# Kernel optimization log

Hardware: AMD Instinct MI355X
Metric: run time of the kernel (lower is better)

The kernel has to match this reference:

```python
import jax, jax.numpy as jnp
import numpy as np

# ---- constants matching init_kwargs ----
NUM_CLASSES = 20
NUM_GRID = 7
NUM_BBOX = 2
IN_SIZE = 448          # image_shapes = (448, 448)
IOU_THRESHOLD = 0.7    # self.num_threshold passed to batched_nms
SCORE_THRESHOLD = 0.1  # boxes[:, -1] > 0.1 reserve mask
M = NUM_GRID * NUM_GRID  # 49 boxes per image
BATCH = 16384


def setup_inputs() -> dict:
    key = jax.random.key(0)
    out_features = M * (NUM_CLASSES + 5 * NUM_BBOX)  # 1470
    x = jax.random.uniform(key, (BATCH, out_features), dtype=jnp.float32)
    return {"x": x}


def _iou_matrix(boxes):
    # boxes: [M, 4] in (x0, y0, x1, y1). Returns [M, M] pairwise IoU.
    area = jnp.clip(boxes[:, 2] - boxes[:, 0], 0) * jnp.clip(boxes[:, 3] - boxes[:, 1], 0)
    lt = jnp.maximum(boxes[:, None, :2], boxes[None, :, :2])   # [M, M, 2]
    rb = jnp.minimum(boxes[:, None, 2:], boxes[None, :, 2:])   # [M, M, 2]
    wh = jnp.clip(rb - lt, 0)
    inter = wh[..., 0] * wh[..., 1]
    union = area[:, None] + area[None, :] - inter
    return inter / jnp.maximum(union, 1e-9)


def _nms_keep(boxes, scores, labels, valid):
    # Per-image class-aware NMS (torchvision batched_nms semantics via coordinate offsets).
    # boxes [M,4], scores [M], labels [M] int, valid [M] bool -> keep mask [M] bool.
    max_coord = jnp.max(boxes)
    offs = labels.astype(boxes.dtype) * (max_coord + 1.0)
    b = boxes + offs[:, None]
    s = jnp.where(valid, scores, -jnp.inf)
    order = jnp.argsort(-s)                 # descending by score, invalid last
    bs = b[order]
    vs = valid[order]
    iou = _iou_matrix(bs)                   # [M, M]
    idx = jnp.arange(M)

    def step(suppressed, i):
        keep_i = vs[i] & ~suppressed[i]
        suppressed = suppressed | (keep_i & (iou[i] > IOU_THRESHOLD) & (idx > i))
        return suppressed, keep_i

    _, keep_sorted = jax.lax.scan(step, jnp.zeros((M,), bool), idx)
    return jnp.zeros((M,), bool).at[order].set(keep_sorted)


def reference(x):
    N = x.shape[0]
    x = x.reshape(N, M, NUM_CLASSES + 5 * NUM_BBOX)
    class_logits = x[..., :NUM_CLASSES]                       # [N, M, C]
    bb = x[..., NUM_CLASSES:].reshape(N, M, NUM_BBOX, 5)      # [N, M, B, 5]
    # pick the bbox with max confidence per cell
    best = jnp.argmax(bb[..., 4], axis=-1)                    # [N, M]
    yolo_bboxes = jnp.take_along_axis(bb, best[..., None, None], axis=2)[:, :, 0, :]  # [N, M, 5]

    probs = jax.nn.softmax(class_logits, axis=-1)
    labels = jnp.argmax(probs, axis=-1)                       # [N, M]

    # boxes_decode: grid offsets (x tiles, y repeats) then cx/cy/w/h -> corners
    g = jnp.arange(NUM_GRID, dtype=x.dtype)
    x_grid = jnp.tile(g, NUM_GRID)                            # [M]
    y_grid = jnp.repeat(g, NUM_GRID)                          # [M]
    cx = (yolo_bboxes[..., 0] + x_grid) / NUM_GRID
    cy = (yolo_bboxes[..., 1] + y_grid) / NUM_GRID
    hw = yolo_bboxes[..., 2] / 2
    hh = yolo_bboxes[..., 3] / 2
    W = jnp.asarray(IN_SIZE, x.dtype)
    H = jnp.asarray(IN_SIZE, x.dtype)
    x0 = (cx - hw) * W
    y0 = (cy - hh) * H
    x1 = (cx + hw) * W
    y1 = (cy + hh) * H
    scores = yolo_bboxes[..., 4]
    reserve_mask = scores > SCORE_THRESHOLD                   # [N, M]

    # clip_boxes_to_image
    x0 = jnp.clip(x0, 0, IN_SIZE); x1 = jnp.clip(x1, 0, IN_SIZE)
    y0 = jnp.clip(y0, 0, IN_SIZE); y1 = jnp.clip(y1, 0, IN_SIZE)
    boxes = jnp.stack([x0, y0, x1, y1], axis=-1)              # [N, M, 4]

    keep_mask = jax.vmap(_nms_keep)(boxes, scores, labels, reserve_mask)  # [N, M]
    return class_logits, yolo_bboxes, boxes, scores, labels, keep_mask, reserve_mask
```

## Files before the change

### kernel.cpp

```cpp
#include <hip/hip_runtime.h>
#include <math.h>

#define NCLS   20
#define MCELLS 49
#define FEAT   30
#define ITEMF  1470

typedef unsigned long long u64;
typedef unsigned int u32;
typedef float f32x4 __attribute__((ext_vector_type(4)));

__device__ __forceinline__ int bcasti(int v, int l) {
  return __builtin_amdgcn_readlane(v, l);
}
__device__ __forceinline__ void nts(float* p, float v) { __builtin_nontemporal_store(v, p); }

__global__ __launch_bounds__(256) void yolo_post(const float* __restrict__ x,
                                                 float* __restrict__ out,
                                                 int N) {
  const int wave = threadIdx.x >> 6;
  const int lane = threadIdx.x & 63;
  const int n = blockIdx.x * 4 + wave;
  if (n >= N) return;

  const float* item = x + (size_t)n * ITEMF;

  const size_t NM = (size_t)N * MCELLS;
  float* out0 = out;
  float* out1 = out0 + NM * 20;
  float* out2 = out1 + NM * 5;
  float* out3 = out2 + NM * 4;
  float* out4 = out3 + NM;
  float* out5 = out4 + NM;
  float* out6 = out5 + NM;

  const int m = lane;
  const bool cellv = (m < MCELLS);

  float2 v[15];
  if (cellv) {
    const float2* Lp = (const float2*)(item + m * FEAT);
#pragma unroll
    for (int j = 0; j < 15; ++j) v[j] = Lp[j];
  } else {
#pragma unroll
    for (int j = 0; j < 15; ++j) v[j] = make_float2(0.f, 0.f);
  }

  {
    float* dst = out0 + (size_t)n * (MCELLS * NCLS);
#pragma unroll
    for (int i = 0; i < 16; ++i) {
      int idx = lane + i * 64;
      if (idx < MCELLS * NCLS) {
        int c = idx / NCLS;
        int k = idx - c * NCLS;
        nts(dst + idx, item[c * FEAT + k]);
      }
    }
  }

  int   labi = 0;
  float conf = 0.f;
  float x0 = 0.f, y0 = 0.f, x1 = 0.f, y1 = 0.f;
  bool  reserve = false;

  if (cellv) {
    float bestv = v[0].x;
    if (v[0].y > bestv) { bestv = v[0].y; labi = 1; }
#pragma unroll
    for (int j = 1; j < 10; ++j) {
      if (v[j].x > bestv) { bestv = v[j].x; labi = 2 * j; }
      if (v[j].y > bestv) { bestv = v[j].y; labi = 2 * j + 1; }
    }

    float c0 = v[12].x, c1 = v[14].y;
    bool sel1 = (c1 > c0);
    float bx = sel1 ? v[12].y : v[10].x;
    float by = sel1 ? v[13].x : v[10].y;
    float bw = sel1 ? v[13].y : v[11].x;
    float bh = sel1 ? v[14].x : v[11].y;
    conf = sel1 ? c1 : c0;

    float xg = (float)(m % 7), yg = (float)(m / 7);
    float cx = (bx + xg) / 7.0f, cy = (by + yg) / 7.0f;
    float hw = bw * 0.5f, hh = bh * 0.5f;
    x0 = fminf(fmaxf((cx - hw) * 448.0f, 0.f), 448.f);
    y0 = fminf(fmaxf((cy - hh) * 448.0f, 0.f), 448.f);
    x1 = fminf(fmaxf((cx + hw) * 448.0f, 0.f), 448.f);
    y1 = fminf(fmaxf((cy + hh) * 448.0f, 0.f), 448.f);
    reserve = (conf > 0.1f);

    size_t ci = (size_t)n * MCELLS + m;
    float* yb = out1 + ci * 5;
    nts(yb + 0, bx); nts(yb + 1, by); nts(yb + 2, bw); nts(yb + 3, bh); nts(yb + 4, conf);
    f32x4 bx4 = { x0, y0, x1, y1 };
    __builtin_nontemporal_store(bx4, (f32x4*)(out2 + ci * 4));
    nts(out3 + ci, conf);
    nts(out4 + ci, (float)labi);
    nts(out6 + ci, reserve ? 1.0f : 0.0f);
  }

  u64 key;
  if (cellv && reserve) {
    u32 sb = __float_as_uint(conf);
    u32 inv = 0x7FFFFFFFu - sb;
    key = ((u64)labi << 37) | ((u64)inv << 6) | (u64)lane;
  } else {
    key = ~0ull;
  }

#pragma unroll
  for (int k = 2; k <= 64; k <<= 1) {
#pragma unroll
    for (int j = k >> 1; j >= 1; j >>= 1) {
      u64 ok = __shfl(key, lane ^ j);
      bool lower = (lane & j) == 0;
      bool asc = (lane & k) == 0;
      if ((key > ok) == (lower == asc)) key = ok;
    }
  }

  const int sid  = (int)(key & 63);
  const int slab = (int)((key >> 37) & 31);

  float gx0 = __shfl(x0, sid), gy0 = __shfl(y0, sid);
  float gx1 = __shfl(x1, sid), gy1 = __shfl(y1, sid);
  float garea = fmaxf(gx1 - gx0, 0.f) * fmaxf(gy1 - gy0, 0.f);

  {
  }
  int prevlab = __shfl(slab, (lane + 63) & 63);
  bool rstart = (lane == 0) || (prevlab != slab);
  u64 S = __ballot(rstart);
  u64 le_mask = (lane == 63) ? ~0ull : ((2ull << lane) - 1ull);
  int st = 63 - __builtin_clzll(S & le_mask);
  u64 gt = (lane == 63) ? 0ull : (S >> (lane + 1));
  int nxt = gt ? (lane + 1 + (int)__builtin_ctzll(gt)) : 64;
  int rl = (slab != 31) ? (nxt - st) : 1;
#pragma unroll
  for (int d2 = 1; d2 < 64; d2 <<= 1) {
    int o = __shfl_xor(rl, d2);
    rl = rl > o ? rl : o;
  }
  const int Dmax = __builtin_amdgcn_readfirstlane(rl);

  u64 rowm = 0;
  for (int d = 1; d < Dmax; ++d) {
    int srcl = (lane + d) & 63;
    int plab = __shfl(slab, srcl);
    float px0 = __shfl(gx0, srcl), py0 = __shfl(gy0, srcl);
    float px1 = __shfl(gx1, srcl), py1 = __shfl(gy1, srcl);
    float pa  = __shfl(garea, srcl);
    bool match = (plab == slab) && (slab != 31) && (lane + d < 64);
    float iw = fmaxf(fminf(px1, gx1) - fmaxf(px0, gx0), 0.f);
    float ih = fmaxf(fminf(py1, gy1) - fmaxf(py0, gy0), 0.f);
    float inter = iw * ih;
    float uni = pa + garea - inter;
    bool ok = match && (inter > 0.7f * fmaxf(uni, 1e-9f));
    rowm |= ok ? (1ull << srcl) : 0ull;
  }

  int V = __popcll(__ballot(key != ~0ull));
  int rlo = (int)(rowm & 0xFFFFFFFFull), rhi = (int)(rowm >> 32);
  u64 remaining = (V >= 64) ? ~0ull : ((1ull << V) - 1ull);
  u64 keep = 0;
  while (remaining) {
    int i = (int)__builtin_ctzll(remaining);
    keep |= 1ull << i;
    u64 rm = ((u64)(u32)bcasti(rhi, i) << 32) | (u32)bcasti(rlo, i);
    remaining &= ~(rm | (1ull << i));
  }

  int kb = (int)((keep >> lane) & 1ull);
  int kf = __builtin_amdgcn_ds_permute(sid << 2, __float_as_int((float)kb));
  if (cellv) nts(out5 + (size_t)n * MCELLS + m, __int_as_float(kf));
}

extern "C" void kernel_launch(void* const* d_in, const int* in_sizes, int n_in,
                              void* d_out, int out_size, void* d_ws, size_t ws_size,
                              hipStream_t stream) {
  const float* x = (const float*)d_in[0];
  float* out = (float*)d_out;
  int N = in_sizes[0] / ITEMF;
  int grid = (N + 3) / 4;
  yolo_post<<<grid, 256, 0, stream>>>(x, out, N);
}
```

Measured before the change: 43.09 us.

## Replace bitonic sort NMS with LDS-based all-pairs suppression and ballot resolution

Drops the 64-lane bitonic sort and sorted-order serial NMS loop. Instead, each lane writes its box and metadata to LDS, tests all 49 boxes for same-class higher-score overlap to build a candidate suppressor mask, and resolves keep decisions with a wave-wide iterative ballot that stops once no undecided boxes remain. This removes the shuffle-heavy sort and the per-kept readlane chain, at the cost of 49 LDS reads per lane and a loop whose iteration count depends on the length of the suppression dependency chain.

Result: slower. 54.72 us (+27.0%).

```diff
diff --git a/kernel.cpp b/kernel.cpp
--- a/kernel.cpp
+++ b/kernel.cpp
@@ -10,9 +10,6 @@
 typedef unsigned int u32;
 typedef float f32x4 __attribute__((ext_vector_type(4)));
 
-__device__ __forceinline__ int bcasti(int v, int l) {
-  return __builtin_amdgcn_readlane(v, l);
-}
 __device__ __forceinline__ void nts(float* p, float v) { __builtin_nontemporal_store(v, p); }
 
 __global__ __launch_bounds__(256) void yolo_post(const float* __restrict__ x,
@@ -21,6 +18,10 @@
   const int wave = threadIdx.x >> 6;
   const int lane = threadIdx.x & 63;
   const int n = blockIdx.x * 4 + wave;
+
+  __shared__ float4 sbox[4][MCELLS];
+  __shared__ float2 smeta[4][MCELLS];
+
   if (n >= N) return;
 
   const float* item = x + (size_t)n * ITEMF;
@@ -99,82 +100,46 @@
     nts(out3 + ci, conf);
     nts(out4 + ci, (float)labi);
     nts(out6 + ci, reserve ? 1.0f : 0.0f);
+
+    sbox[wave][m]  = make_float4(x0, y0, x1, y1);
+    smeta[wave][m] = make_float2(conf, __int_as_float(labi));
+  }
+  __threadfence_block();
+
+  const float area_i = fmaxf(x1 - x0, 0.f) * fmaxf(y1 - y0, 0.f);
+  u64 cand = 0;
+#pragma unroll 7
+  for (int j = 0; j < MCELLS; ++j) {
+    float4 bj = sbox[wave][j];
+    float2 mj = smeta[wave][j];
+    float cj = mj.x;
+    int  labj = __float_as_int(mj.y);
+    bool prec = (labj == labi) && (cj > 0.1f) &&
+                ((cj > conf) || ((cj == conf) && (j < m)));
+    float aj = fmaxf(bj.z - bj.x, 0.f) * fmaxf(bj.w - bj.y, 0.f);
+    float iw = fminf(bj.z, x1) - fmaxf(bj.x, x0);
+    float ih = fminf(bj.w, y1) - fmaxf(bj.y, y0);
+    float inter = fmaxf(iw, 0.f) * fmaxf(ih, 0.f);
+    float uni = aj + area_i - inter;
+    bool sup = prec && (inter > 0.7f * fmaxf(uni, 1e-9f));
+    cand |= sup ? (1ull << j) : 0ull;
+  }
+  if (!(cellv && reserve)) cand = 0;
+
+  u64 valid = __ballot(cellv && reserve);
+  u64 undecided = valid;
+  u64 kept = 0;
+  bool meValid = (cellv && reserve);
+  while (undecided) {
+    bool meUnd = meValid && ((undecided >> lane) & 1ull);
+    bool ready = meUnd && ((cand & undecided) == 0ull);
+    u64 readyb = __ballot(ready);
+    u64 keptb  = __ballot(ready && ((cand & kept) == 0ull));
+    kept |= keptb;
+    undecided &= ~readyb;
   }
 
-  u64 key;
-  if (cellv && reserve) {
-    u32 sb = __float_as_uint(conf);
-    u32 inv = 0x7FFFFFFFu - sb;
-    key = ((u64)labi << 37) | ((u64)inv << 6) | (u64)lane;
-  } else {
-    key = ~0ull;
-  }
-
-#pragma unroll
-  for (int k = 2; k <= 64; k <<= 1) {
-#pragma unroll
-    for (int j = k >> 1; j >= 1; j >>= 1) {
-      u64 ok = __shfl(key, lane ^ j);
-      bool lower = (lane & j) == 0;
-      bool asc = (lane & k) == 0;
-      if ((key > ok) == (lower == asc)) key = ok;
-    }
-  }
-
-  const int sid  = (int)(key & 63);
-  const int slab = (int)((key >> 37) & 31);
-
-  float gx0 = __shfl(x0, sid), gy0 = __shfl(y0, sid);
-  float gx1 = __shfl(x1, sid), gy1 = __shfl(y1, sid);
-  float garea = fmaxf(gx1 - gx0, 0.f) * fmaxf(gy1 - gy0, 0.f);
-
-  {
-  }
-  int prevlab = __shfl(slab, (lane + 63) & 63);
-  bool rstart = (lane == 0) || (prevlab != slab);
-  u64 S = __ballot(rstart);
-  u64 le_mask = (lane == 63) ? ~0ull : ((2ull << lane) - 1ull);
-  int st = 63 - __builtin_clzll(S & le_mask);
-  u64 gt = (lane == 63) ? 0ull : (S >> (lane + 1));
-  int nxt = gt ? (lane + 1 + (int)__builtin_ctzll(gt)) : 64;
-  int rl = (slab != 31) ? (nxt - st) : 1;
-#pragma unroll
-  for (int d2 = 1; d2 < 64; d2 <<= 1) {
-    int o = __shfl_xor(rl, d2);
-    rl = rl > o ? rl : o;
-  }
-  const int Dmax = __builtin_amdgcn_readfirstlane(rl);
-
-  u64 rowm = 0;
-  for (int d = 1; d < Dmax; ++d) {
-    int srcl = (lane + d) & 63;
-    int plab = __shfl(slab, srcl);
-    float px0 = __shfl(gx0, srcl), py0 = __shfl(gy0, srcl);
-    float px1 = __shfl(gx1, srcl), py1 = __shfl(gy1, srcl);
-    float pa  = __shfl(garea, srcl);
-    bool match = (plab == slab) && (slab != 31) && (lane + d < 64);
-    float iw = fmaxf(fminf(px1, gx1) - fmaxf(px0, gx0), 0.f);
-    float ih = fmaxf(fminf(py1, gy1) - fmaxf(py0, gy0), 0.f);
-    float inter = iw * ih;
-    float uni = pa + garea - inter;
-    bool ok = match && (inter > 0.7f * fmaxf(uni, 1e-9f));
-    rowm |= ok ? (1ull << srcl) : 0ull;
-  }
-
-  int V = __popcll(__ballot(key != ~0ull));
-  int rlo = (int)(rowm & 0xFFFFFFFFull), rhi = (int)(rowm >> 32);
-  u64 remaining = (V >= 64) ? ~0ull : ((1ull << V) - 1ull);
-  u64 keep = 0;
-  while (remaining) {
-    int i = (int)__builtin_ctzll(remaining);
-    keep |= 1ull << i;
-    u64 rm = ((u64)(u32)bcasti(rhi, i) << 32) | (u32)bcasti(rlo, i);
-    remaining &= ~(rm | (1ull << i));
-  }
-
-  int kb = (int)((keep >> lane) & 1ull);
-  int kf = __builtin_amdgcn_ds_permute(sid << 2, __float_as_int((float)kb));
-  if (cellv) nts(out5 + (size_t)n * MCELLS + m, __int_as_float(kf));
+  if (cellv) nts(out5 + (size_t)n * MCELLS + m, (float)((kept >> lane) & 1ull));
 }
 
 extern "C" void kernel_launch(void* const* d_in, const int* in_sizes, int n_in,
```
